# Optimization experiments

Hardware: AMD Instinct MI355X
Metric: run time of the kernel (lower is better)

The kernel has to match this reference:

```python
import jax, jax.numpy as jnp
import numpy as np

C = 256   # descriptor_dim
H = 4     # num_heads
D = C // H  # head_dim = 64
B, N = 8, 2048


def _conv1x1(x, w, b):
    # 1x1 Conv1d == per-position linear over channels: x [B,C,N], w [O,C], b [O]
    return jnp.einsum('oc,bcn->bon', w, x) + b[None, :, None]


def setup_inputs() -> dict:
    key = jax.random.key(0)
    ks = jax.random.split(key, 11)
    s = 1.0 / np.sqrt(C)
    return {
        'query': jax.random.normal(ks[0], (B, C, N), dtype=jnp.float32),
        'key':   jax.random.normal(ks[1], (B, C, N), dtype=jnp.float32),
        'value': jax.random.normal(ks[2], (B, C, N), dtype=jnp.float32),
        'wq': jax.random.normal(ks[3], (C, C), dtype=jnp.float32) * s,
        'bq': jax.random.normal(ks[4], (C,), dtype=jnp.float32) * s,
        'wk': jax.random.normal(ks[5], (C, C), dtype=jnp.float32) * s,
        'bk': jax.random.normal(ks[6], (C,), dtype=jnp.float32) * s,
        'wv': jax.random.normal(ks[7], (C, C), dtype=jnp.float32) * s,
        'bv': jax.random.normal(ks[8], (C,), dtype=jnp.float32) * s,
        'wm': jax.random.normal(ks[9], (C, C), dtype=jnp.float32) * s,
        'bm': jax.random.normal(ks[10], (C,), dtype=jnp.float32) * s,
    }


def reference(query, key, value, wq, bq, wk, bk, wv, bv, wm, bm):
    b = query.shape[0]
    # project then view channels as (head_dim, num_heads) -- matches torch .view order
    q = _conv1x1(query, wq, bq).reshape(b, D, H, -1)   # [B,D,H,N]
    k = _conv1x1(key,   wk, bk).reshape(b, D, H, -1)   # [B,D,H,M]
    v = _conv1x1(value, wv, bv).reshape(b, D, H, -1)   # [B,D,H,M]
    scores = jnp.einsum('bdhn,bdhm->bhnm', q, k) / (D ** 0.5)
    probs = jax.nn.softmax(scores, axis=-1)            # [B,H,N,M]
    out = jnp.einsum('bhnm,bdhm->bdhn', probs, v)      # [B,D,H,N]
    out = out.reshape(b, D * H, -1)                    # [B,C,N]
    return _conv1x1(out, wm, bm)
```

## Files before the change

kernel.cpp:

```cpp
#include <hip/hip_runtime.h>
#include <hip/hip_bf16.h>

typedef float f32x4 __attribute__((ext_vector_type(4)));
typedef float f32x16 __attribute__((ext_vector_type(16)));
typedef __bf16 bf16x8 __attribute__((ext_vector_type(8)));
typedef __bf16 bf16x4 __attribute__((ext_vector_type(4)));
typedef unsigned int uint2v __attribute__((ext_vector_type(2)));
typedef unsigned int u32;

constexpr int B_ = 8, C_ = 256, N_ = 2048, H_ = 4, D_ = 64;
constexpr int BH_ = B_ * H_;
constexpr size_t PER_ = (size_t)BH_ * N_ * D_;
constexpr float LOG2E = 1.44269504088896340736f;

static __device__ __forceinline__ float fast_exp2(float x) {
#if __has_builtin(__builtin_amdgcn_exp2f)
  return __builtin_amdgcn_exp2f(x);
#else
  return exp2f(x);
#endif
}

static __device__ __forceinline__ void* swz(void* base, int row, int cb) {
  return (char*)base + row * 128 + (cb ^ ((row & 7) << 4));
}
static __device__ __forceinline__ const void* swz(const void* base, int row, int cb) {
  return (const char*)base + row * 128 + (cb ^ ((row & 7) << 4));
}

static __device__ __forceinline__ void gload16(void* lds, const void* g) {
  __builtin_amdgcn_global_load_lds(
      (const __attribute__((address_space(1))) u32*)g,
      (__attribute__((address_space(3))) u32*)lds, 16, 0, 0);
}

struct W4 {
  const float* s0; const float* s1; const float* s2; const float* s3;
  __bf16* d0; __bf16* d1; __bf16* d2; __bf16* d3;
};

__global__ __launch_bounds__(256) void wcvt_kernel(W4 p) {
  const int m = blockIdx.y;
  const float* src = m == 0 ? p.s0 : m == 1 ? p.s1 : m == 2 ? p.s2 : p.s3;
  __bf16* dst = m == 0 ? p.d0 : m == 1 ? p.d1 : m == 2 ? p.d2 : p.d3;
  const int f = blockIdx.x * 256 + threadIdx.x;
  const int o_blk = f >> 9;
  const int ks = (f >> 6) & 7;
  const int lane = f & 63;
  const int row = o_blk * 16 + (lane & 15);
  const int kbase = ks * 32 + (lane >> 4) * 8;
  bf16x8 v;
  if (m == 3) {
    for (int e = 0; e < 8; e++) {
      const int k = kbase + e;
      const int c = ((k & 63) << 2) | (k >> 6);
      v[e] = (__bf16)src[row * 256 + c];
    }
  } else {
    const int srow = ((row & 63) << 2) | (row >> 6);
    const float* s = src + srow * 256 + kbase;
    float4 a = *(const float4*)s;
    float4 b = *(const float4*)(s + 4);
    v[0] = (__bf16)a.x; v[1] = (__bf16)a.y; v[2] = (__bf16)a.z; v[3] = (__bf16)a.w;
    v[4] = (__bf16)b.x; v[5] = (__bf16)b.y; v[6] = (__bf16)b.z; v[7] = (__bf16)b.w;
  }
  *(bf16x8*)&dst[(size_t)f * 8] = v;
}

__global__ __launch_bounds__(256) void qkv_fused_kernel(
    const float* __restrict__ xq, const float* __restrict__ xk,
    const float* __restrict__ xv, const __bf16* __restrict__ wfq,
    const __bf16* __restrict__ wfk, const __bf16* __restrict__ wfv,
    const float* __restrict__ bq, const float* __restrict__ bk,
    const float* __restrict__ bv, __bf16* __restrict__ oq,
    char* __restrict__ oksw, char* __restrict__ ovsw) {
  __shared__ __bf16 xlds[64][264];

  const int m = blockIdx.x >> 8;
  int inner = blockIdx.x & 255;
  inner = (inner & 7) * 32 + (inner >> 3);
  const int b = inner >> 5, nb = inner & 31;
  const int n0 = nb * 64;

  const float* xf = m == 0 ? xq : m == 1 ? xk : xv;
  const __bf16* wf = m == 0 ? wfq : m == 1 ? wfk : wfv;
  const float* bias = m == 0 ? bq : m == 1 ? bk : bv;
  const float scale = m == 0 ? 0.125f * LOG2E : 1.0f;

  const int t = threadIdx.x;
  {
    const int kl = t >> 4;
    const int nl = (t & 15) * 4;
    const float* src = xf + (size_t)b * C_ * N_ + n0 + nl;
    for (int it = 0; it < 16; it++) {
      const int k = it * 16 + kl;
      float4 f = *(const float4*)(src + (size_t)k * N_);
      xlds[nl + 0][k] = (__bf16)f.x;
      xlds[nl + 1][k] = (__bf16)f.y;
      xlds[nl + 2][k] = (__bf16)f.z;
      xlds[nl + 3][k] = (__bf16)f.w;
    }
  }
  __syncthreads();

  const int lane = t & 63, wvv = t >> 6;
  const int wm = wvv >> 1, wn = wvv & 1;
  const int l15 = lane & 15, lg = lane >> 4;

  f32x4 acc[8][2] = {};

  for (int ks = 0; ks < 8; ks++) {
    bf16x8 bfr[2];
    for (int ni = 0; ni < 2; ni++)
      bfr[ni] = *(const bf16x8*)&xlds[wn * 32 + ni * 16 + l15][ks * 32 + lg * 8];
    for (int mi = 0; mi < 8; mi++) {
      bf16x8 af = *(const bf16x8*)&wf[(((size_t)(wm * 8 + mi) * 8 + ks) * 64 + lane) * 8];
      acc[mi][0] = __builtin_amdgcn_mfma_f32_16x16x32_bf16(af, bfr[0], acc[mi][0], 0, 0, 0);
      acc[mi][1] = __builtin_amdgcn_mfma_f32_16x16x32_bf16(af, bfr[1], acc[mi][1], 0, 0, 0);
    }
  }

  for (int mi = 0; mi < 8; mi++) {
    const int h = wm * 2 + (mi >> 2);
    const int d0 = (mi & 3) * 16 + 4 * lg;
    for (int ni = 0; ni < 2; ni++) {
      const int n = n0 + wn * 32 + ni * 16 + l15;
      const size_t tbase = ((size_t)(b * H_ + h) * (N_ / 64) + (n >> 6)) * 8192;
      if (m == 0) {
        bf16x4 o4;
        for (int r = 0; r < 4; r++)
          o4[r] = (__bf16)((acc[mi][ni][r] + bias[((d0 + r) << 2) | h]) * scale);
        *(bf16x4*)&oq[((size_t)(b * H_ + h) * N_ + n) * D_ + d0] = o4;
      } else if (m == 1) {
        bf16x4 o4;
        for (int r = 0; r < 4; r++)
          o4[r] = (__bf16)(acc[mi][ni][r] + bias[((d0 + r) << 2) | h]);
        *(bf16x4*)swz(oksw + tbase, n & 63, 2 * d0) = o4;
      } else {
        for (int r = 0; r < 4; r++)
          *(__bf16*)swz(ovsw + tbase, d0 + r, 2 * (n & 63)) =
              (__bf16)(acc[mi][ni][r] + bias[((d0 + r) << 2) | h]);
      }
    }
  }
}

__global__ __launch_bounds__(256) void final_proj_kernel(
    const __bf16* __restrict__ xb, const __bf16* __restrict__ wf,
    const float* __restrict__ bias, float* __restrict__ out) {
  const int bid = blockIdx.x;
  const int wid = (bid & 7) * 128 + (bid >> 3);
  const int o_t = wid & 3;
  const int nb = (wid >> 2) & 31;
  const int b = wid >> 7;
  const int o0 = o_t * 64, n0 = nb * 64;
  const int t = threadIdx.x, lane = t & 63;
  const int wvv = t >> 6, wm = wvv >> 1, wn = wvv & 1;
  const int l15 = lane & 15, lg = lane >> 4;
  const int nbase = n0 + wn * 32 + l15;

  f32x4 acc[2][2] = {};

  for (int ks = 0; ks < 8; ks++) {
    bf16x8 af[2];
    for (int mi = 0; mi < 2; mi++)
      af[mi] = *(const bf16x8*)&wf[(((size_t)(o_t * 4 + wm * 2 + mi) * 8 + ks) * 64 + lane) * 8];
    bf16x8 bfr[2];
    const size_t bh = (size_t)(b * H_ + (ks >> 1));
    const int d0 = (ks & 1) * 32 + lg * 8;
    for (int ni = 0; ni < 2; ni++)
      bfr[ni] = *(const bf16x8*)&xb[(bh * N_ + nbase + ni * 16) * D_ + d0];
    for (int mi = 0; mi < 2; mi++)
      for (int ni = 0; ni < 2; ni++)
        acc[mi][ni] = __builtin_amdgcn_mfma_f32_16x16x32_bf16(
            af[mi], bfr[ni], acc[mi][ni], 0, 0, 0);
  }

  for (int mi = 0; mi < 2; mi++) {
    for (int r = 0; r < 4; r++) {
      const int och = o0 + wm * 32 + mi * 16 + 4 * lg + r;
      const float bv_ = bias[och];
      for (int ni = 0; ni < 2; ni++) {
        const int n = n0 + wn * 32 + ni * 16 + l15;
        out[((size_t)b * C_ + och) * N_ + n] = acc[mi][ni][r] + bv_;
      }
    }
  }
}

template <int SPLIT>
__global__ __launch_bounds__(512) void attn_kernel(
    const __bf16* __restrict__ qb, const char* __restrict__ kbsw,
    const char* __restrict__ vtsw, __bf16* __restrict__ pO,
    float* __restrict__ lbuf) {
  __shared__ char smem[32768];

  const int t = threadIdx.x, lane = t & 63, wv = t >> 6;
  const int l31 = lane & 31, hi = lane >> 5;

  const int bid = blockIdx.x;
  const int per_xcd = (256 * SPLIT) / 8;
  const int wid = (bid & 7) * per_xcd + (bid >> 3);
  const int bh = wid / (8 * SPLIT);
  const int rem = wid % (8 * SPLIT);
  const int qt = rem & 7;
  const int s = rem >> 3;
  const int qn = qt * 256 + wv * 32;
  constexpr int NT = N_ / SPLIT / 64;
  const int jt0 = s * NT;

  const char* ktiles = kbsw + (size_t)bh * (N_ / 64) * 8192;
  const char* vtiles = vtsw + (size_t)bh * (N_ / 64) * 8192;

  const __bf16* qrow = qb + ((size_t)bh * N_ + qn + l31) * D_;
  bf16x8 qf[4];
#pragma unroll
  for (int i = 0; i < 4; i++) qf[i] = *(const bf16x8*)(qrow + i * 16 + hi * 8);

  auto stage = [&](int jt_g, int bb) {
    gload16(smem + bb * 8192 + t * 16, ktiles + (size_t)jt_g * 8192 + t * 16);
    gload16(smem + 16384 + bb * 8192 + t * 16,
            vtiles + (size_t)jt_g * 8192 + t * 16);
  };

  stage(jt0, 0);
  __syncthreads();

  f32x16 o0 = {}, o1 = {};
  float la0 = 0.f, la1 = 0.f, la2 = 0.f, la3 = 0.f;
  int cur = 0;

  for (int jt = 0; jt < NT; jt++) {
    if (jt + 1 < NT) stage(jt0 + jt + 1, cur ^ 1);
    const char* kc = smem + cur * 8192;
    const char* vc = smem + 16384 + cur * 8192;

    f32x16 s0 = {}, s1 = {};
    __builtin_amdgcn_s_setprio(1);
#pragma unroll
    for (int i = 0; i < 4; i++) {
      bf16x8 kf = *(const bf16x8*)swz(kc, l31, i * 32 + hi * 16);
      s0 = __builtin_amdgcn_mfma_f32_32x32x16_bf16(kf, qf[i], s0, 0, 0, 0);
    }
#pragma unroll
    for (int i = 0; i < 4; i++) {
      bf16x8 kf = *(const bf16x8*)swz(kc, 32 + l31, i * 32 + hi * 16);
      s1 = __builtin_amdgcn_mfma_f32_32x32x16_bf16(kf, qf[i], s1, 0, 0, 0);
    }
    __builtin_amdgcn_s_setprio(0);

#pragma unroll
    for (int sub = 0; sub < 2; sub++) {
      const f32x16 sv = sub ? s1 : s0;
      float pr[16];
#pragma unroll
      for (int r = 0; r < 16; r++) pr[r] = fast_exp2(sv[r]);
      la0 += pr[0] + pr[4] + pr[8] + pr[12];
      la1 += pr[1] + pr[5] + pr[9] + pr[13];
      la2 += pr[2] + pr[6] + pr[10] + pr[14];
      la3 += pr[3] + pr[7] + pr[11] + pr[15];
      unsigned w[8];
#pragma unroll
      for (int g = 0; g < 8; g++) {
        union { __bf16 h[2]; unsigned u; } cv;
        cv.h[0] = (__bf16)pr[2 * g];
        cv.h[1] = (__bf16)pr[2 * g + 1];
        w[g] = cv.u;
      }
      uint2v r0 = __builtin_amdgcn_permlane32_swap(w[0], w[2], false, false);
      uint2v r1 = __builtin_amdgcn_permlane32_swap(w[1], w[3], false, false);
      uint2v r2 = __builtin_amdgcn_permlane32_swap(w[4], w[6], false, false);
      uint2v r3 = __builtin_amdgcn_permlane32_swap(w[5], w[7], false, false);
      union { unsigned u[4]; bf16x8 v; } f0 = {{r0.x, r1.x, r0.y, r1.y}};
      union { unsigned u[4]; bf16x8 v; } f1 = {{r2.x, r3.x, r2.y, r3.y}};
      const int scb = sub * 64;
      __builtin_amdgcn_s_setprio(1);
      {
        bf16x8 vf = *(const bf16x8*)swz(vc, l31, scb + hi * 16);
        o0 = __builtin_amdgcn_mfma_f32_32x32x16_bf16(vf, f0.v, o0, 0, 0, 0);
        vf = *(const bf16x8*)swz(vc, l31, scb + 32 + hi * 16);
        o0 = __builtin_amdgcn_mfma_f32_32x32x16_bf16(vf, f1.v, o0, 0, 0, 0);
        vf = *(const bf16x8*)swz(vc, 32 + l31, scb + hi * 16);
        o1 = __builtin_amdgcn_mfma_f32_32x32x16_bf16(vf, f0.v, o1, 0, 0, 0);
        vf = *(const bf16x8*)swz(vc, 32 + l31, scb + 32 + hi * 16);
        o1 = __builtin_amdgcn_mfma_f32_32x32x16_bf16(vf, f1.v, o1, 0, 0, 0);
      }
      __builtin_amdgcn_s_setprio(0);
    }

    __syncthreads();
    cur ^= 1;
  }

  float la = la0 + la1 + la2 + la3;
  la += __shfl_xor(la, 32);
  const float scl = (SPLIT == 1) ? 1.f / la : 1.f;

  if constexpr (SPLIT > 1) {
    if (hi == 0)
      lbuf[(size_t)s * BH_ * N_ + (size_t)bh * N_ + qn + l31] = la;
  }

  char* ep = smem + wv * 4096;
#pragma unroll
  for (int dt = 0; dt < 2; dt++) {
    const f32x16 o = dt ? o1 : o0;
#pragma unroll
    for (int g = 0; g < 4; g++) {
      bf16x4 o4;
#pragma unroll
      for (int j = 0; j < 4; j++) o4[j] = (__bf16)(o[4 * g + j] * scl);
      *(bf16x4*)swz(ep, l31, dt * 64 + 16 * g + 8 * hi) = o4;
    }
  }
  asm volatile("" ::: "memory");
  {
    __bf16* dst = pO + (size_t)s * PER_ + ((size_t)bh * N_ + qn) * D_;
#pragma unroll
    for (int i = 0; i < 4; i++) {
      const int row = i * 8 + (lane >> 3);
      uint4 v = *(const uint4*)swz(ep, row, (lane & 7) * 16);
      *(uint4*)((char*)dst + i * 1024 + lane * 16) = v;
    }
  }
}

__global__ __launch_bounds__(256) void combine_kernel(
    const __bf16* __restrict__ p0, const __bf16* __restrict__ p1,
    const float* __restrict__ l0, const float* __restrict__ l1,
    __bf16* __restrict__ outp) {
  const size_t idx8 = (size_t)blockIdx.x * 256 + threadIdx.x;
  const size_t nidx = idx8 >> 3;
  bf16x8 a = *(const bf16x8*)&p0[idx8 * 8];
  bf16x8 b = *(const bf16x8*)&p1[idx8 * 8];
  const float inv = 1.f / (l0[nidx] + l1[nidx]);
  bf16x8 r;
#pragma unroll
  for (int e = 0; e < 8; e++) r[e] = (__bf16)(((float)a[e] + (float)b[e]) * inv);
  *(bf16x8*)&outp[idx8 * 8] = r;
}

extern "C" void kernel_launch(void* const* d_in, const int* in_sizes, int n_in,
                              void* d_out, int out_size, void* d_ws,
                              size_t ws_size, hipStream_t stream) {
  const float* query = (const float*)d_in[0];
  const float* key_ = (const float*)d_in[1];
  const float* value = (const float*)d_in[2];
  const float* wq = (const float*)d_in[3];
  const float* bq = (const float*)d_in[4];
  const float* wk = (const float*)d_in[5];
  const float* bk = (const float*)d_in[6];
  const float* wv = (const float*)d_in[7];
  const float* bv = (const float*)d_in[8];
  const float* wm = (const float*)d_in[9];
  const float* bm = (const float*)d_in[10];

  __bf16* qb = (__bf16*)d_ws;
  char* kbsw = (char*)(qb + PER_);
  char* vtsw = kbsw + PER_ * 2;
  __bf16* p0 = (__bf16*)(vtsw + PER_ * 2);
  __bf16* p1 = p0 + PER_;
  float* lbuf = (float*)(p1 + PER_);
  __bf16* wfq = (__bf16*)(lbuf + 2 * BH_ * N_);
  __bf16* wfk = wfq + 65536;
  __bf16* wfv = wfk + 65536;
  __bf16* wfm = wfv + 65536;

  const size_t need_split = (size_t)((char*)(wfm + 65536) - (char*)d_ws);
  const bool use_split = ws_size >= need_split;

  dim3 blk(256);
  W4 wp{wq, wk, wv, wm, wfq, wfk, wfv, wfm};
  if (!use_split) {
    wfq = p1; wfk = wfq + 65536; wfv = wfk + 65536; wfm = wfv + 65536;
    wp = W4{wq, wk, wv, wm, wfq, wfk, wfv, wfm};
  }
  wcvt_kernel<<<dim3(32, 4), blk, 0, stream>>>(wp);

  qkv_fused_kernel<<<768, blk, 0, stream>>>(query, key_, value, wfq, wfk, wfv,
                                            bq, bk, bv, qb, kbsw, vtsw);
  if (use_split) {
    attn_kernel<2><<<512, dim3(512), 0, stream>>>(qb, kbsw, vtsw, p0, lbuf);
    combine_kernel<<<2048, blk, 0, stream>>>(p0, p1, lbuf, lbuf + BH_ * N_, p0);
  } else {
    attn_kernel<1><<<256, dim3(512), 0, stream>>>(qb, kbsw, vtsw, p0, nullptr);
  }
  final_proj_kernel<<<1024, blk, 0, stream>>>(p0, wfm, bm, (float*)d_out);
}
```

Before: 98.42 us.

## Fuse split combine into final projection, triple-buffer attention, pack QKV LDS writes

Removes the separate combine kernel and instead merges the two split-attention partials and their normalizers inside the final projection's operand loads. This saves one launch and a full read/write pass over the partial output. The attention kernel moves from double to triple-buffered K/V staging with explicit vmcnt waits, so loads run two tiles ahead. The QKV projection now writes pairs of bf16 into LDS as 32-bit stores instead of scalar 16-bit stores. The costs are extra LDS per attention block (48KB), and each final-projection block re-reads both partials for its output tile, which is redundant across the four output-channel tiles.

```diff
diff --git a/kernel.cpp b/kernel.cpp
--- a/kernel.cpp
+++ b/kernel.cpp
@@ -89,16 +89,22 @@
 
   const int t = threadIdx.x;
   {
-    const int kl = t >> 4;
-    const int nl = (t & 15) * 4;
+    const int kl = t & 15;
+    const int nl = (t >> 4) * 4;
     const float* src = xf + (size_t)b * C_ * N_ + n0 + nl;
-    for (int it = 0; it < 16; it++) {
-      const int k = it * 16 + kl;
-      float4 f = *(const float4*)(src + (size_t)k * N_);
-      xlds[nl + 0][k] = (__bf16)f.x;
-      xlds[nl + 1][k] = (__bf16)f.y;
-      xlds[nl + 2][k] = (__bf16)f.z;
-      xlds[nl + 3][k] = (__bf16)f.w;
+    for (int kp = 0; kp < 8; kp++) {
+      const int k = kp * 32 + kl * 2;
+      float4 f0 = *(const float4*)(src + (size_t)k * N_);
+      float4 f1 = *(const float4*)(src + (size_t)(k + 1) * N_);
+      union { __bf16 h[2]; u32 u; } c0, c1, c2, c3;
+      c0.h[0] = (__bf16)f0.x; c0.h[1] = (__bf16)f1.x;
+      c1.h[0] = (__bf16)f0.y; c1.h[1] = (__bf16)f1.y;
+      c2.h[0] = (__bf16)f0.z; c2.h[1] = (__bf16)f1.z;
+      c3.h[0] = (__bf16)f0.w; c3.h[1] = (__bf16)f1.w;
+      *(u32*)&xlds[nl + 0][k] = c0.u;
+      *(u32*)&xlds[nl + 1][k] = c1.u;
+      *(u32*)&xlds[nl + 2][k] = c2.u;
+      *(u32*)&xlds[nl + 3][k] = c3.u;
     }
   }
   __syncthreads();
@@ -145,9 +151,12 @@
   }
 }
 
+template <int COMB>
 __global__ __launch_bounds__(256) void final_proj_kernel(
-    const __bf16* __restrict__ xb, const __bf16* __restrict__ wf,
-    const float* __restrict__ bias, float* __restrict__ out) {
+    const __bf16* __restrict__ p0, const __bf16* __restrict__ p1,
+    const float* __restrict__ l0, const float* __restrict__ l1,
+    const __bf16* __restrict__ wf, const float* __restrict__ bias,
+    float* __restrict__ out) {
   const int bid = blockIdx.x;
   const int wid = (bid & 7) * 128 + (bid >> 3);
   const int o_t = wid & 3;
@@ -159,6 +168,15 @@
   const int l15 = lane & 15, lg = lane >> 4;
   const int nbase = n0 + wn * 32 + l15;
 
+  float inv[2][4];
+  if constexpr (COMB) {
+    for (int ni = 0; ni < 2; ni++)
+      for (int h = 0; h < 4; h++) {
+        const size_t bhn = (size_t)(b * H_ + h) * N_ + nbase + ni * 16;
+        inv[ni][h] = 1.f / (l0[bhn] + l1[bhn]);
+      }
+  }
+
   f32x4 acc[2][2] = {};
 
   for (int ks = 0; ks < 8; ks++) {
@@ -166,10 +184,24 @@
     for (int mi = 0; mi < 2; mi++)
       af[mi] = *(const bf16x8*)&wf[(((size_t)(o_t * 4 + wm * 2 + mi) * 8 + ks) * 64 + lane) * 8];
     bf16x8 bfr[2];
-    const size_t bh = (size_t)(b * H_ + (ks >> 1));
+    const int h = ks >> 1;
+    const size_t bh = (size_t)(b * H_ + h);
     const int d0 = (ks & 1) * 32 + lg * 8;
-    for (int ni = 0; ni < 2; ni++)
-      bfr[ni] = *(const bf16x8*)&xb[(bh * N_ + nbase + ni * 16) * D_ + d0];
+    for (int ni = 0; ni < 2; ni++) {
+      const size_t off = (bh * N_ + nbase + ni * 16) * D_ + d0;
+      bf16x8 a = *(const bf16x8*)&p0[off];
+      if constexpr (COMB) {
+        bf16x8 bb = *(const bf16x8*)&p1[off];
+        const float iv = inv[ni][h];
+        bf16x8 r;
+#pragma unroll
+        for (int e = 0; e < 8; e++)
+          r[e] = (__bf16)(((float)a[e] + (float)bb[e]) * iv);
+        bfr[ni] = r;
+      } else {
+        bfr[ni] = a;
+      }
+    }
     for (int mi = 0; mi < 2; mi++)
       for (int ni = 0; ni < 2; ni++)
         acc[mi][ni] = __builtin_amdgcn_mfma_f32_16x16x32_bf16(
@@ -193,7 +225,7 @@
     const __bf16* __restrict__ qb, const char* __restrict__ kbsw,
     const char* __restrict__ vtsw, __bf16* __restrict__ pO,
     float* __restrict__ lbuf) {
-  __shared__ char smem[32768];
+  __shared__ char smem[49152];
 
   const int t = threadIdx.x, lane = t & 63, wv = t >> 6;
   const int l31 = lane & 31, hi = lane >> 5;
@@ -219,21 +251,28 @@
 
   auto stage = [&](int jt_g, int bb) {
     gload16(smem + bb * 8192 + t * 16, ktiles + (size_t)jt_g * 8192 + t * 16);
-    gload16(smem + 16384 + bb * 8192 + t * 16,
+    gload16(smem + 24576 + bb * 8192 + t * 16,
             vtiles + (size_t)jt_g * 8192 + t * 16);
   };
 
   stage(jt0, 0);
-  __syncthreads();
+  if (NT > 1) stage(jt0 + 1, 1);
+  asm volatile("s_waitcnt vmcnt(2)" ::: "memory");
+  __builtin_amdgcn_sched_barrier(0);
+  __builtin_amdgcn_s_barrier();
+  __builtin_amdgcn_sched_barrier(0);
 
   f32x16 o0 = {}, o1 = {};
   float la0 = 0.f, la1 = 0.f, la2 = 0.f, la3 = 0.f;
   int cur = 0;
 
   for (int jt = 0; jt < NT; jt++) {
-    if (jt + 1 < NT) stage(jt0 + jt + 1, cur ^ 1);
+    if (jt + 2 < NT) {
+      int sb = cur + 2; if (sb >= 3) sb -= 3;
+      stage(jt0 + jt + 2, sb);
+    }
     const char* kc = smem + cur * 8192;
-    const char* vc = smem + 16384 + cur * 8192;
+    const char* vc = smem + 24576 + cur * 8192;
 
     f32x16 s0 = {}, s1 = {};
     __builtin_amdgcn_s_setprio(1);
@@ -288,8 +327,17 @@
       __builtin_amdgcn_s_setprio(0);
     }
 
-    __syncthreads();
-    cur ^= 1;
+    if (jt + 1 < NT) {
+      if (jt + 2 < NT) {
+        asm volatile("s_waitcnt vmcnt(2)" ::: "memory");
+      } else {
+        asm volatile("s_waitcnt vmcnt(0)" ::: "memory");
+      }
+      __builtin_amdgcn_sched_barrier(0);
+      __builtin_amdgcn_s_barrier();
+      __builtin_amdgcn_sched_barrier(0);
+    }
+    cur++; if (cur == 3) cur = 0;
   }
 
   float la = la0 + la1 + la2 + la3;
@@ -301,6 +349,7 @@
       lbuf[(size_t)s * BH_ * N_ + (size_t)bh * N_ + qn + l31] = la;
   }
 
+  __syncthreads();
   char* ep = smem + wv * 4096;
 #pragma unroll
   for (int dt = 0; dt < 2; dt++) {
@@ -323,21 +372,6 @@
       *(uint4*)((char*)dst + i * 1024 + lane * 16) = v;
     }
   }
-}
-
-__global__ __launch_bounds__(256) void combine_kernel(
-    const __bf16* __restrict__ p0, const __bf16* __restrict__ p1,
-    const float* __restrict__ l0, const float* __restrict__ l1,
-    __bf16* __restrict__ outp) {
-  const size_t idx8 = (size_t)blockIdx.x * 256 + threadIdx.x;
-  const size_t nidx = idx8 >> 3;
-  bf16x8 a = *(const bf16x8*)&p0[idx8 * 8];
-  bf16x8 b = *(const bf16x8*)&p1[idx8 * 8];
-  const float inv = 1.f / (l0[nidx] + l1[nidx]);
-  bf16x8 r;
-#pragma unroll
-  for (int e = 0; e < 8; e++) r[e] = (__bf16)(((float)a[e] + (float)b[e]) * inv);
-  *(bf16x8*)&outp[idx8 * 8] = r;
 }
 
 extern "C" void kernel_launch(void* const* d_in, const int* in_sizes, int n_in,
@@ -381,9 +415,11 @@
                                             bq, bk, bv, qb, kbsw, vtsw);
   if (use_split) {
     attn_kernel<2><<<512, dim3(512), 0, stream>>>(qb, kbsw, vtsw, p0, lbuf);
-    combine_kernel<<<2048, blk, 0, stream>>>(p0, p1, lbuf, lbuf + BH_ * N_, p0);
+    final_proj_kernel<1><<<1024, blk, 0, stream>>>(
+        p0, p1, lbuf, lbuf + BH_ * N_, wfm, bm, (float*)d_out);
   } else {
     attn_kernel<1><<<256, dim3(512), 0, stream>>>(qb, kbsw, vtsw, p0, nullptr);
-  }
-  final_proj_kernel<<<1024, blk, 0, stream>>>(p0, wfm, bm, (float*)d_out);
-}
+    final_proj_kernel<0><<<1024, blk, 0, stream>>>(
+        p0, p0, nullptr, nullptr, wfm, bm, (float*)d_out);
+  }
+}
```

Result: no change. 100.1 us (+1.7%).
